# Kernel tuning notes

Measured on AMD Instinct MI355X. Metric: run time of the kernel, lower is better.

The kernel has to match this reference:

```python
import jax, jax.numpy as jnp
import numpy as np

# static config (mirrors init_kwargs)
F_T, S = 8, 24            # video_shape = (F_T, S, S)
K, DIL = 3, 1             # kernel_size, dilation (same for all 3 axes)
HEADS, DHEAD, DIM = 8, 64, 512
INNER = HEADS * DHEAD
PAD = DIL * (K - 1)       # causal: pad 2 at the FRONT of each spatial axis
KJ = K ** 3               # 27 neighbors per query
N_VID = F_T * S * S       # 4608 video tokens


def causal_pad(t):
    # t: [B, D, F, S, S] -> pad front of f/h/w axes (torch F.pad (PAD*?,0) causal layout)
    return jnp.pad(t, ((0, 0), (0, 0), (PAD, 0), (PAD, 0), (PAD, 0)))


def unfold3d(t):
    # torch unfoldNd equivalent. t: [B, D, F+PAD, S+PAD, S+PAD]
    # returns [B, N_VID, KJ, D]; kernel offsets ordered (kf, kh, kw) w fastest,
    # matching torch unfold's channel-major / kernel-minor layout after the
    # rearrange 'b (d j) i -> b i j d'.
    sl = []
    for i in range(K):
        for j in range(K):
            for kk in range(K):
                sl.append(t[:, :, i * DIL:i * DIL + F_T,
                                  j * DIL:j * DIL + S,
                                  kk * DIL:kk * DIL + S])
    u = jnp.stack(sl, axis=2)                      # [B, D, KJ, F, S, S]
    B, D = t.shape[0], t.shape[1]
    u = u.reshape(B, D, KJ, N_VID)
    return jnp.transpose(u, (0, 3, 2, 1))          # [B, N_VID, KJ, D]


def make_mask():
    # True where the neighbor falls into zero padding (out-of-range / future under causal pad)
    ones = jnp.ones((1, 1, F_T, S, S), jnp.float32)
    u = unfold3d(causal_pad(ones))[0, :, :, 0]     # [N_VID, KJ]
    m = u == 0.0
    return jnp.pad(m, ((0, 0), (1, 0)), constant_values=False)  # bos col never masked


def stable_softmax(t, alpha=32.0 ** 2):
    t = t / alpha
    t = t - jax.lax.stop_gradient(jnp.max(t, axis=-1, keepdims=True))
    return jax.nn.softmax(t * alpha, axis=-1)


def setup_inputs() -> dict:
    key = jax.random.key(0)
    ks = jax.random.split(key, 9)
    return {
        "x": jax.random.normal(ks[0], (1, N_VID + 1, DIM), jnp.float32),
        "Wq": jax.random.normal(ks[1], (DIM, INNER), jnp.float32) * 0.02,
        "Wkv": jax.random.normal(ks[2], (DIM, 2 * INNER), jnp.float32) * 0.02,
        "W_th": jax.random.normal(ks[3], (HEADS, HEADS), jnp.float32) * 0.2,
        "Wout": jax.random.normal(ks[4], (INNER, DIM), jnp.float32) * 0.02,
        "bout": jax.random.normal(ks[5], (DIM,), jnp.float32) * 0.02,
        "ax1": jax.random.normal(ks[6], (K, HEADS), jnp.float32),
        "ax2": jax.random.normal(ks[7], (K, HEADS), jnp.float32),
        "ax3": jax.random.normal(ks[8], (K, HEADS), jnp.float32),
    }


def reference(x, Wq, Wkv, W_th, Wout, bout, ax1, ax2, ax3):
    b, n, _ = x.shape                       # b=1, n = 1 + N_VID (no extra padding)
    h, d = HEADS, DHEAD
    scale = d ** -0.5

    q = x @ Wq
    k, v = jnp.split(x @ Wkv, 2, axis=-1)

    def to_heads(t):  # 'b n (h d) -> (b h) n d'
        return t.reshape(b, n, h, d).transpose(0, 2, 1, 3).reshape(b * h, n, d)

    q, k, v = map(to_heads, (q, k, v))
    q = q[:, 1:] * scale                    # drop bos query
    k_bos, v_bos = k[:, :1], v[:, :1]       # [bh, 1, d]
    k, v = k[:, 1:], v[:, 1:]

    def to_vid(t):  # 'b (f h w) d -> b d f h w'
        return t.reshape(b * h, F_T, S, S, d).transpose(0, 4, 1, 2, 3)

    ku = unfold3d(causal_pad(to_vid(k)))    # [bh, N, KJ, d]
    vu = unfold3d(causal_pad(to_vid(v)))
    N = ku.shape[1]

    kb = jnp.broadcast_to(k_bos[:, :, None, :], (b * h, N, 1, d))
    vb = jnp.broadcast_to(v_bos[:, :, None, :], (b * h, N, 1, d))
    ku = jnp.concatenate([kb, ku], axis=2)  # [bh, N, KJ+1, d]
    vu = jnp.concatenate([vb, vu], axis=2)

    sim = jnp.einsum('bid,bijd->bij', q, ku)                 # [bh, N, KJ+1]

    # axial relative position bias over the 3x3x3 kernel, pad 0 for bos column
    rel = (ax1[:, None, None, :] + ax2[None, :, None, :] + ax3[None, None, :, :])
    rel = rel.reshape(KJ, h)                                 # [27, h]
    bias = jnp.pad(rel.T[:, None, :], ((0, 0), (0, 0), (1, 0)))  # [h, 1, KJ+1]

    sim = sim.reshape(b, h, N, KJ + 1) + bias[None]
    mask = make_mask()                                       # [N, KJ+1]
    sim = jnp.where(mask[None, None], -jnp.finfo(sim.dtype).max, sim)

    attn = stable_softmax(sim)                               # [b, h, N, KJ+1]
    attn = jnp.einsum('hg,bgij->bhij', W_th, attn)           # talking heads 1x1 conv

    out = jnp.einsum('bhij,bhijd->bhid', attn, vu.reshape(b, h, N, KJ + 1, d))
    out = jnp.concatenate([v_bos.reshape(b, h, 1, d), out], axis=2)  # re-attach bos value
    out = out.transpose(0, 2, 1, 3).reshape(b, n, h * d)     # '(b h) n d -> b n (h d)'
    return out @ Wout + bout
```

## Files before the change

### kernel.cpp

```cpp
#include <hip/hip_runtime.h>
#include <hip/hip_bf16.h>


constexpr int TFR   = 8;
constexpr int SDIM  = 24;
constexpr int NVID  = TFR * SDIM * SDIM;
constexpr int NTOK  = NVID + 1;
constexpr int NH    = 8;
constexpr int DM    = 512;
constexpr int NJ    = 28;

typedef __attribute__((ext_vector_type(8))) short bf16x8;
typedef __attribute__((ext_vector_type(8))) unsigned short ushort8;
typedef __attribute__((ext_vector_type(4))) float f32x4;

typedef const __attribute__((address_space(1))) unsigned int* gas_ptr;
typedef __attribute__((address_space(3))) unsigned int* las_ptr;

__device__ __forceinline__ float bf2f(unsigned short u) {
    return __uint_as_float((unsigned)u << 16);
}
__device__ __forceinline__ unsigned short f2bf(float f) {
    __hip_bfloat16 h = __float2bfloat16(f);
    return reinterpret_cast<unsigned short&>(h);
}

__global__ __launch_bounds__(256)
void prep_w(const float* __restrict__ Wq, const float* __restrict__ Wkv,
            const float* __restrict__ Wout, const float* __restrict__ x,
            __hip_bfloat16* __restrict__ Wqkvt, __hip_bfloat16* __restrict__ Woutt,
            __hip_bfloat16* __restrict__ xb)
{
    const int tid = threadIdx.x;
    int tb = blockIdx.x;

    if (tb >= 1024) {
        const size_t base = (size_t)(tb - 1024) * 2048 + (size_t)tid * 8;
        if (base < (size_t)NTOK * DM) {
            const float4 f0 = *(const float4*)(x + base);
            const float4 f1 = *(const float4*)(x + base + 4);
            unsigned short v[8] = { f2bf(f0.x), f2bf(f0.y), f2bf(f0.z), f2bf(f0.w),
                                    f2bf(f1.x), f2bf(f1.y), f2bf(f1.z), f2bf(f1.w) };
            *(ushort8*)(xb + base) = *(const ushort8*)v;
        }
        return;
    }

    __shared__ float t[32][33];
    const float* W; __hip_bfloat16* Wt; int Nd, tX, rowOff;
    if (tb < 256)      { W = Wq;   Wt = Wqkvt; Nd = 512;  tX = 16; rowOff = 0;   }
    else if (tb < 768) { tb -= 256; W = Wkv;  Wt = Wqkvt; Nd = 1024; tX = 32; rowOff = 512; }
    else               { tb -= 768; W = Wout; Wt = Woutt; Nd = 512;  tX = 16; rowOff = 0;   }
    const int n0 = (tb % tX) * 32, k0 = (tb / tX) * 32;
    const int r  = tid >> 3;
    const int c4 = (tid & 7) * 4;
    const float4 v = *(const float4*)(W + (size_t)(k0 + r) * Nd + n0 + c4);
    t[r][c4 + 0] = v.x; t[r][c4 + 1] = v.y; t[r][c4 + 2] = v.z; t[r][c4 + 3] = v.w;
    __syncthreads();
    #pragma unroll
    for (int j = 0; j < 4; ++j)
        Wt[(size_t)(rowOff + n0 + r) * 512 + k0 + c4 + j] = __float2bfloat16(t[c4 + j][r]);
}

__global__ __launch_bounds__(256)
void gemm_qkv(const __hip_bfloat16* __restrict__ Ab, const __hip_bfloat16* __restrict__ Bt,
              float* __restrict__ Cq, __hip_bfloat16* __restrict__ Ckv, int M)
{
    constexpr int BM = 128, BN = 128, BK = 64, K = 512;
    __shared__ __align__(16) short As[BM * BK];
    __shared__ __align__(16) short Bs[BN * BK];

    const int tid  = threadIdx.x;
    const int bid  = blockIdx.x;
    const int xcd  = bid & 7, pos = bid >> 3;
    const int L    = (xcd < 4) ? xcd * 56 + pos : 224 + (xcd - 4) * 55 + pos;
    const int m0   = (L / 12) * BM;
    const int n0   = (L % 12) * BN;

    const int lane = tid & 63;
    const int wave = tid >> 6;
    const int wm   = (wave >> 1) * 64;
    const int wn   = (wave & 1) * 64;
    const int col  = lane & 15;
    const int quad = lane >> 4;

    f32x4 acc[4][4] = {};

    for (int k0 = 0; k0 < K; k0 += BK) {
        #pragma unroll
        for (int it = 0; it < 4; ++it) {
            const int idx = it * 256 + tid;
            const int r   = idx >> 3;
            const int u   = (idx & 7) ^ (r & 7);
            const int gm  = (m0 + r < M) ? (m0 + r) : (M - 1);
            const __hip_bfloat16* gp = Ab + (size_t)gm * K + k0 + u * 8;
            __builtin_amdgcn_global_load_lds(
                (gas_ptr)gp, (las_ptr)&As[(it * 256 + wave * 64) * 8], 16, 0, 0);
        }
        #pragma unroll
        for (int it = 0; it < 4; ++it) {
            const int idx = it * 256 + tid;
            const int r   = idx >> 3;
            const int u   = (idx & 7) ^ (r & 7);
            const __hip_bfloat16* gp = Bt + (size_t)(n0 + r) * K + k0 + u * 8;
            __builtin_amdgcn_global_load_lds(
                (gas_ptr)gp, (las_ptr)&Bs[(it * 256 + wave * 64) * 8], 16, 0, 0);
        }
        __syncthreads();

        #pragma unroll
        for (int ks = 0; ks < 2; ++ks) {
            bf16x8 af[4], bfr[4];
            #pragma unroll
            for (int mt = 0; mt < 4; ++mt) {
                const int r = wm + mt * 16 + col;
                const int u = (ks * 4 + quad) ^ (r & 7);
                af[mt] = *(const bf16x8*)(&As[r * BK + u * 8]);
            }
            #pragma unroll
            for (int nt = 0; nt < 4; ++nt) {
                const int r = wn + nt * 16 + col;
                const int u = (ks * 4 + quad) ^ (r & 7);
                bfr[nt] = *(const bf16x8*)(&Bs[r * BK + u * 8]);
            }
            #pragma unroll
            for (int mt = 0; mt < 4; ++mt)
                #pragma unroll
                for (int nt = 0; nt < 4; ++nt)
                    acc[mt][nt] = __builtin_amdgcn_mfma_f32_16x16x32_bf16(
                        af[mt], bfr[nt], acc[mt][nt], 0, 0, 0);
        }
        __syncthreads();
    }

    const bool isQ = (n0 < 512);
    #pragma unroll
    for (int mt = 0; mt < 4; ++mt) {
        #pragma unroll
        for (int r = 0; r < 4; ++r) {
            const int row = m0 + wm + mt * 16 + quad * 4 + r;
            if (row >= M) continue;
            #pragma unroll
            for (int nt = 0; nt < 4; ++nt) {
                const int cg = n0 + wn + nt * 16 + col;
                const float v = acc[mt][nt][r];
                if (isQ) Cq[(size_t)row * 512 + cg] = v * 0.125f;
                else     Ckv[(size_t)row * 1024 + (cg - 512)] = __float2bfloat16(v);
            }
        }
    }
}

__global__ __launch_bounds__(256)
void gemm_out(const __hip_bfloat16* __restrict__ A, const __hip_bfloat16* __restrict__ Bt,
              float* __restrict__ C, int M, const float* __restrict__ bias)
{
    constexpr int BM = 64, BN = 64, BK = 64, K = 512;
    __shared__ __align__(16) short As[BM * BK];
    __shared__ __align__(16) short Bs[BN * BK];

    const int tid  = threadIdx.x;
    const int bid  = blockIdx.x;
    const int L    = (bid & 7) * 73 + (bid >> 3);
    const int m0   = (L >> 3) * BM;
    const int n0   = (L & 7) * BN;
    const int lane = tid & 63;
    const int wave = tid >> 6;
    const int wm   = (wave >> 1) * 32;
    const int wn   = (wave & 1) * 32;
    const int col  = lane & 15;
    const int quad = lane >> 4;

    f32x4 acc[2][2] = {};

    for (int k0 = 0; k0 < K; k0 += BK) {
        #pragma unroll
        for (int it = 0; it < 2; ++it) {
            const int idx = it * 256 + tid;
            const int r   = idx >> 3;
            const int u   = (idx & 7) ^ (r & 7);
            const int gm  = (m0 + r < M) ? (m0 + r) : (M - 1);
            const __hip_bfloat16* gp = A + (size_t)gm * K + k0 + u * 8;
            __builtin_amdgcn_global_load_lds(
                (gas_ptr)gp, (las_ptr)&As[(it * 256 + wave * 64) * 8], 16, 0, 0);
        }
        #pragma unroll
        for (int it = 0; it < 2; ++it) {
            const int idx = it * 256 + tid;
            const int r   = idx >> 3;
            const int u   = (idx & 7) ^ (r & 7);
            const __hip_bfloat16* gp = Bt + (size_t)(n0 + r) * K + k0 + u * 8;
            __builtin_amdgcn_global_load_lds(
                (gas_ptr)gp, (las_ptr)&Bs[(it * 256 + wave * 64) * 8], 16, 0, 0);
        }
        __syncthreads();

        #pragma unroll
        for (int ks = 0; ks < 2; ++ks) {
            bf16x8 af[2], bfr[2];
            #pragma unroll
            for (int mt = 0; mt < 2; ++mt) {
                const int r = wm + mt * 16 + col;
                const int u = (ks * 4 + quad) ^ (r & 7);
                af[mt] = *(const bf16x8*)(&As[r * BK + u * 8]);
            }
            #pragma unroll
            for (int nt = 0; nt < 2; ++nt) {
                const int r = wn + nt * 16 + col;
                const int u = (ks * 4 + quad) ^ (r & 7);
                bfr[nt] = *(const bf16x8*)(&Bs[r * BK + u * 8]);
            }
            #pragma unroll
            for (int mt = 0; mt < 2; ++mt)
                #pragma unroll
                for (int nt = 0; nt < 2; ++nt)
                    acc[mt][nt] = __builtin_amdgcn_mfma_f32_16x16x32_bf16(
                        af[mt], bfr[nt], acc[mt][nt], 0, 0, 0);
        }
        __syncthreads();
    }

    #pragma unroll
    for (int mt = 0; mt < 2; ++mt) {
        #pragma unroll
        for (int r = 0; r < 4; ++r) {
            const int row = m0 + wm + mt * 16 + quad * 4 + r;
            if (row >= M) continue;
            #pragma unroll
            for (int nt = 0; nt < 2; ++nt) {
                const int cg = n0 + wn + nt * 16 + col;
                C[(size_t)row * 512 + cg] = acc[mt][nt][r] + bias[cg];
            }
        }
    }
}

__global__ __launch_bounds__(256)
void attn_v2(const float* __restrict__ Q, const __hip_bfloat16* __restrict__ KVb,
             __hip_bfloat16* __restrict__ O,
             const float* __restrict__ W_th,
             const float* __restrict__ ax1, const float* __restrict__ ax2,
             const float* __restrict__ ax3)
{
    __shared__ float attn_s[4][NH * NJ];
    __shared__ float mixed_s[4][NH * NJ];

    const int tid  = threadIdx.x;
    const int wave = tid >> 6;
    const int lane = tid & 63;
    const int g    = lane >> 3;
    const int s    = lane & 7;
    const int bsw  = (blockIdx.x & 7) * (NVID / 4 / 8) + (blockIdx.x >> 3);
    const int i    = __builtin_amdgcn_readfirstlane(bsw * 4 + (tid >> 6));
    const int qrow = i + 1;

    const int t  = i / (SDIM * SDIM);
    const int rm = i % (SDIM * SDIM);
    const int y  = rm / SDIM;
    const int x  = rm % SDIM;

    float qf[8];
    {
        const float4 q0 = *(const float4*)(Q + (size_t)qrow * DM + lane * 8);
        const float4 q1 = *(const float4*)(Q + (size_t)qrow * DM + lane * 8 + 4);
        qf[0] = q0.x; qf[1] = q0.y; qf[2] = q0.z; qf[3] = q0.w;
        qf[4] = q1.x; qf[5] = q1.y; qf[6] = q1.z; qf[7] = q1.w;
    }
    float a1[3], a2[3], a3[3];
    #pragma unroll
    for (int d = 0; d < 3; ++d) {
        a1[d] = ax1[d * NH + g];
        a2[d] = ax2[d * NH + g];
        a3[d] = ax3[d * NH + g];
    }

    float sim[NJ];
    #pragma unroll
    for (int j = 0; j < NJ; ++j) {
        int row; bool valid; float bias;
        if (j == 0) { row = 0; valid = true; bias = 0.f; }
        else {
            const int jp = j - 1;
            const int di = jp / 9, dj = (jp / 3) % 3, dk = jp % 3;
            const int tt = t + di - 2, yy = y + dj - 2, xx = x + dk - 2;
            valid = (tt >= 0) && (yy >= 0) && (xx >= 0);
            row = 1 + tt * SDIM * SDIM + yy * SDIM + xx;
            bias = a1[di] + a2[dj] + a3[dk];
        }
        if (valid) {
            const ushort8 kv = *(const ushort8*)(KVb + (size_t)row * 1024 + lane * 8);
            float p = 0.f;
            #pragma unroll
            for (int e = 0; e < 8; ++e) p += bf2f(kv[e]) * qf[e];
            p += __shfl_xor(p, 1);
            p += __shfl_xor(p, 2);
            p += __shfl_xor(p, 4);
            sim[j] = p + bias;
        } else {
            sim[j] = -1e30f;
        }
    }

    float m = -1e30f;
    #pragma unroll
    for (int j = 0; j < NJ; ++j) m = fmaxf(m, sim[j]);
    float ssum = 0.f;
    #pragma unroll
    for (int j = 0; j < NJ; ++j) { sim[j] = __expf(sim[j] - m); ssum += sim[j]; }
    const float inv = 1.f / ssum;
    #pragma unroll
    for (int j = 0; j < NJ; ++j) sim[j] *= inv;

    if (s == 0) {
        #pragma unroll
        for (int u = 0; u < 7; ++u) {
            f32x4 v4 = { sim[4*u], sim[4*u+1], sim[4*u+2], sim[4*u+3] };
            *(f32x4*)(&attn_s[wave][g * NJ + 4 * u]) = v4;
        }
    }
    __syncthreads();

    if (tid < NH * NJ) {
        const int h = tid / NJ, j = tid % NJ;
        #pragma unroll
        for (int q = 0; q < 4; ++q) {
            float acc = 0.f;
            #pragma unroll
            for (int gg = 0; gg < NH; ++gg)
                acc += W_th[h * NH + gg] * attn_s[q][gg * NJ + j];
            mixed_s[q][h * NJ + j] = acc;
        }
    }
    __syncthreads();

    float acc8[8] = {};
    #pragma unroll
    for (int j = 0; j < NJ; ++j) {
        int row; bool valid;
        if (j == 0) { row = 0; valid = true; }
        else {
            const int jp = j - 1;
            const int di = jp / 9, dj = (jp / 3) % 3, dk = jp % 3;
            const int tt = t + di - 2, yy = y + dj - 2, xx = x + dk - 2;
            valid = (tt >= 0) && (yy >= 0) && (xx >= 0);
            row = 1 + tt * SDIM * SDIM + yy * SDIM + xx;
        }
        if (valid) {
            const ushort8 vv = *(const ushort8*)(KVb + (size_t)row * 1024 + 512 + lane * 8);
            const float w = mixed_s[wave][g * NJ + j];
            #pragma unroll
            for (int e = 0; e < 8; ++e) acc8[e] += w * bf2f(vv[e]);
        }
    }

    unsigned short o[8];
    #pragma unroll
    for (int e = 0; e < 8; ++e) o[e] = f2bf(acc8[e]);
    *(ushort8*)(O + (size_t)qrow * DM + lane * 8) = *(const ushort8*)o;

    if (i == 0) {
        const ushort8 vb = *(const ushort8*)(KVb + 512 + lane * 8);
        *(ushort8*)(O + lane * 8) = vb;
    }
}

extern "C" void kernel_launch(void* const* d_in, const int* in_sizes, int n_in,
                              void* d_out, int out_size, void* d_ws, size_t ws_size,
                              hipStream_t stream)
{
    const float* x    = (const float*)d_in[0];
    const float* Wq   = (const float*)d_in[1];
    const float* Wkv  = (const float*)d_in[2];
    const float* W_th = (const float*)d_in[3];
    const float* Wout = (const float*)d_in[4];
    const float* bout = (const float*)d_in[5];
    const float* ax1  = (const float*)d_in[6];
    const float* ax2  = (const float*)d_in[7];
    const float* ax3  = (const float*)d_in[8];
    float* out = (float*)d_out;

    char* p = (char*)d_ws;
    float* Qf = (float*)p;                       p += (size_t)NTOK * DM * 4;
    __hip_bfloat16* KVb   = (__hip_bfloat16*)p;  p += (size_t)NTOK * 2 * DM * 2;
    __hip_bfloat16* Ob    = (__hip_bfloat16*)p;  p += (size_t)NTOK * DM * 2;
    __hip_bfloat16* Wqkvt = (__hip_bfloat16*)p;  p += (size_t)3 * DM * DM * 2;
    __hip_bfloat16* Woutt = (__hip_bfloat16*)p;  p += (size_t)DM * DM * 2;
    __hip_bfloat16* xb    = (__hip_bfloat16*)p;  p += (size_t)NTOK * DM * 2;

    const dim3 blk(256);

    prep_w<<<2177, blk, 0, stream>>>(Wq, Wkv, Wout, x, Wqkvt, Woutt, xb);

    gemm_qkv<<<444, blk, 0, stream>>>(xb, Wqkvt, Qf, KVb, NTOK);

    attn_v2<<<dim3(NVID / 4), blk, 0, stream>>>(Qf, KVb, Ob, W_th, ax1, ax2, ax3);

    gemm_out<<<584, blk, 0, stream>>>(Ob, Woutt, out, NTOK, bout);
}
```

Before: 131.1 us.

## Double-buffer LDS tiles in QKV and output GEMMs to overlap loads

Both GEMM kernels now keep two LDS buffers per operand. The next K-tile is issued with global_load_lds into the spare buffer while MFMAs run on the current one, which is meant to hide global-load latency behind compute. LDS use per block doubles, which can lower occupancy, and the loop keeps a single end-of-iteration barrier, so correctness depends on that barrier also waiting for the async LDS loads.

```diff
diff --git a/kernel.cpp b/kernel.cpp
--- a/kernel.cpp
+++ b/kernel.cpp
@@ -67,8 +67,8 @@
               float* __restrict__ Cq, __hip_bfloat16* __restrict__ Ckv, int M)
 {
     constexpr int BM = 128, BN = 128, BK = 64, K = 512;
-    __shared__ __align__(16) short As[BM * BK];
-    __shared__ __align__(16) short Bs[BN * BK];
+    __shared__ __align__(16) short As[2][BM * BK];
+    __shared__ __align__(16) short Bs[2][BN * BK];
 
     const int tid  = threadIdx.x;
     const int bid  = blockIdx.x;
@@ -86,7 +86,7 @@
 
     f32x4 acc[4][4] = {};
 
-    for (int k0 = 0; k0 < K; k0 += BK) {
+    auto stage = [&](int buf, int k0) {
         #pragma unroll
         for (int it = 0; it < 4; ++it) {
             const int idx = it * 256 + tid;
@@ -95,7 +95,7 @@
             const int gm  = (m0 + r < M) ? (m0 + r) : (M - 1);
             const __hip_bfloat16* gp = Ab + (size_t)gm * K + k0 + u * 8;
             __builtin_amdgcn_global_load_lds(
-                (gas_ptr)gp, (las_ptr)&As[(it * 256 + wave * 64) * 8], 16, 0, 0);
+                (gas_ptr)gp, (las_ptr)&As[buf][(it * 256 + wave * 64) * 8], 16, 0, 0);
         }
         #pragma unroll
         for (int it = 0; it < 4; ++it) {
@@ -104,9 +104,17 @@
             const int u   = (idx & 7) ^ (r & 7);
             const __hip_bfloat16* gp = Bt + (size_t)(n0 + r) * K + k0 + u * 8;
             __builtin_amdgcn_global_load_lds(
-                (gas_ptr)gp, (las_ptr)&Bs[(it * 256 + wave * 64) * 8], 16, 0, 0);
-        }
-        __syncthreads();
+                (gas_ptr)gp, (las_ptr)&Bs[buf][(it * 256 + wave * 64) * 8], 16, 0, 0);
+        }
+    };
+
+    stage(0, 0);
+    __syncthreads();
+
+    #pragma unroll 2
+    for (int t = 0; t < K / BK; ++t) {
+        const int cur = t & 1;
+        if (t + 1 < K / BK) stage(cur ^ 1, (t + 1) * BK);
 
         #pragma unroll
         for (int ks = 0; ks < 2; ++ks) {
@@ -115,13 +123,13 @@
             for (int mt = 0; mt < 4; ++mt) {
                 const int r = wm + mt * 16 + col;
                 const int u = (ks * 4 + quad) ^ (r & 7);
-                af[mt] = *(const bf16x8*)(&As[r * BK + u * 8]);
+                af[mt] = *(const bf16x8*)(&As[cur][r * BK + u * 8]);
             }
             #pragma unroll
             for (int nt = 0; nt < 4; ++nt) {
                 const int r = wn + nt * 16 + col;
                 const int u = (ks * 4 + quad) ^ (r & 7);
-                bfr[nt] = *(const bf16x8*)(&Bs[r * BK + u * 8]);
+                bfr[nt] = *(const bf16x8*)(&Bs[cur][r * BK + u * 8]);
             }
             #pragma unroll
             for (int mt = 0; mt < 4; ++mt)
@@ -156,8 +164,8 @@
               float* __restrict__ C, int M, const float* __restrict__ bias)
 {
     constexpr int BM = 64, BN = 64, BK = 64, K = 512;
-    __shared__ __align__(16) short As[BM * BK];
-    __shared__ __align__(16) short Bs[BN * BK];
+    __shared__ __align__(16) short As[2][BM * BK];
+    __shared__ __align__(16) short Bs[2][BN * BK];
 
     const int tid  = threadIdx.x;
     const int bid  = blockIdx.x;
@@ -173,7 +181,7 @@
 
     f32x4 acc[2][2] = {};
 
-    for (int k0 = 0; k0 < K; k0 += BK) {
+    auto stage = [&](int buf, int k0) {
         #pragma unroll
         for (int it = 0; it < 2; ++it) {
             const int idx = it * 256 + tid;
@@ -182,7 +190,7 @@
             const int gm  = (m0 + r < M) ? (m0 + r) : (M - 1);
             const __hip_bfloat16* gp = A + (size_t)gm * K + k0 + u * 8;
             __builtin_amdgcn_global_load_lds(
-                (gas_ptr)gp, (las_ptr)&As[(it * 256 + wave * 64) * 8], 16, 0, 0);
+                (gas_ptr)gp, (las_ptr)&As[buf][(it * 256 + wave * 64) * 8], 16, 0, 0);
         }
         #pragma unroll
         for (int it = 0; it < 2; ++it) {
@@ -191,9 +199,17 @@
             const int u   = (idx & 7) ^ (r & 7);
             const __hip_bfloat16* gp = Bt + (size_t)(n0 + r) * K + k0 + u * 8;
             __builtin_amdgcn_global_load_lds(
-                (gas_ptr)gp, (las_ptr)&Bs[(it * 256 + wave * 64) * 8], 16, 0, 0);
-        }
-        __syncthreads();
+                (gas_ptr)gp, (las_ptr)&Bs[buf][(it * 256 + wave * 64) * 8], 16, 0, 0);
+        }
+    };
+
+    stage(0, 0);
+    __syncthreads();
+
+    #pragma unroll 2
+    for (int t = 0; t < K / BK; ++t) {
+        const int cur = t & 1;
+        if (t + 1 < K / BK) stage(cur ^ 1, (t + 1) * BK);
 
         #pragma unroll
         for (int ks = 0; ks < 2; ++ks) {
@@ -202,13 +218,13 @@
             for (int mt = 0; mt < 2; ++mt) {
                 const int r = wm + mt * 16 + col;
                 const int u = (ks * 4 + quad) ^ (r & 7);
-                af[mt] = *(const bf16x8*)(&As[r * BK + u * 8]);
+                af[mt] = *(const bf16x8*)(&As[cur][r * BK + u * 8]);
             }
             #pragma unroll
             for (int nt = 0; nt < 2; ++nt) {
                 const int r = wn + nt * 16 + col;
                 const int u = (ks * 4 + quad) ^ (r & 7);
-                bfr[nt] = *(const bf16x8*)(&Bs[r * BK + u * 8]);
+                bfr[nt] = *(const bf16x8*)(&Bs[cur][r * BK + u * 8]);
             }
             #pragma unroll
             for (int mt = 0; mt < 2; ++mt)
```

After: 132.2 us. About the same (+0.8%).

## Fuse all four stages into one persistent cooperative kernel with grid syncs

Applied to the files above, without the earlier changes.

Replaces the four separate launches (weight/x prep, QKV GEMM, neighborhood attention, output GEMM) with a single persistent cooperative kernel. Blocks loop over virtual block indices for each stage and separate the stages with grid.sync. The aim is to remove per-launch overhead and inter-kernel gaps. In exchange, stages become grid-strided loops with a grid size set by occupancy, launch_bounds now asks for 3 blocks per CU, the XCD-aware block swizzles are dropped, and the extra __syncthreads and grid barriers add their own cost.

```diff
diff --git a/kernel.cpp b/kernel.cpp
--- a/kernel.cpp
+++ b/kernel.cpp
@@ -1,5 +1,8 @@
 #include <hip/hip_runtime.h>
 #include <hip/hip_bf16.h>
+#include <hip/hip_cooperative_groups.h>
+
+namespace cg = cooperative_groups;
 
 
 constexpr int TFR   = 8;
@@ -25,342 +28,336 @@
     return reinterpret_cast<unsigned short&>(h);
 }
 
-__global__ __launch_bounds__(256)
-void prep_w(const float* __restrict__ Wq, const float* __restrict__ Wkv,
-            const float* __restrict__ Wout, const float* __restrict__ x,
-            __hip_bfloat16* __restrict__ Wqkvt, __hip_bfloat16* __restrict__ Woutt,
-            __hip_bfloat16* __restrict__ xb)
+__global__ __launch_bounds__(256, 3)
+void fused_all(const float* __restrict__ x,   const float* __restrict__ Wq,
+               const float* __restrict__ Wkv,  const float* __restrict__ W_th,
+               const float* __restrict__ Wout, const float* __restrict__ bout,
+               const float* __restrict__ ax1,  const float* __restrict__ ax2,
+               const float* __restrict__ ax3,  float* __restrict__ out,
+               float* __restrict__ Qf, __hip_bfloat16* __restrict__ KVb,
+               __hip_bfloat16* __restrict__ Ob, __hip_bfloat16* __restrict__ Wqkvt,
+               __hip_bfloat16* __restrict__ Woutt, __hip_bfloat16* __restrict__ xb)
 {
-    const int tid = threadIdx.x;
-    int tb = blockIdx.x;
-
-    if (tb >= 1024) {
-        const size_t base = (size_t)(tb - 1024) * 2048 + (size_t)tid * 8;
-        if (base < (size_t)NTOK * DM) {
-            const float4 f0 = *(const float4*)(x + base);
-            const float4 f1 = *(const float4*)(x + base + 4);
-            unsigned short v[8] = { f2bf(f0.x), f2bf(f0.y), f2bf(f0.z), f2bf(f0.w),
-                                    f2bf(f1.x), f2bf(f1.y), f2bf(f1.z), f2bf(f1.w) };
-            *(ushort8*)(xb + base) = *(const ushort8*)v;
-        }
-        return;
-    }
-
-    __shared__ float t[32][33];
-    const float* W; __hip_bfloat16* Wt; int Nd, tX, rowOff;
-    if (tb < 256)      { W = Wq;   Wt = Wqkvt; Nd = 512;  tX = 16; rowOff = 0;   }
-    else if (tb < 768) { tb -= 256; W = Wkv;  Wt = Wqkvt; Nd = 1024; tX = 32; rowOff = 512; }
-    else               { tb -= 768; W = Wout; Wt = Woutt; Nd = 512;  tX = 16; rowOff = 0;   }
-    const int n0 = (tb % tX) * 32, k0 = (tb / tX) * 32;
-    const int r  = tid >> 3;
-    const int c4 = (tid & 7) * 4;
-    const float4 v = *(const float4*)(W + (size_t)(k0 + r) * Nd + n0 + c4);
-    t[r][c4 + 0] = v.x; t[r][c4 + 1] = v.y; t[r][c4 + 2] = v.z; t[r][c4 + 3] = v.w;
-    __syncthreads();
-    #pragma unroll
-    for (int j = 0; j < 4; ++j)
-        Wt[(size_t)(rowOff + n0 + r) * 512 + k0 + c4 + j] = __float2bfloat16(t[c4 + j][r]);
-}
-
-__global__ __launch_bounds__(256)
-void gemm_qkv(const __hip_bfloat16* __restrict__ Ab, const __hip_bfloat16* __restrict__ Bt,
-              float* __restrict__ Cq, __hip_bfloat16* __restrict__ Ckv, int M)
-{
-    constexpr int BM = 128, BN = 128, BK = 64, K = 512;
-    __shared__ __align__(16) short As[BM * BK];
-    __shared__ __align__(16) short Bs[BN * BK];
-
+    __shared__ __align__(16) char smem[32768];
     const int tid  = threadIdx.x;
-    const int bid  = blockIdx.x;
-    const int xcd  = bid & 7, pos = bid >> 3;
-    const int L    = (xcd < 4) ? xcd * 56 + pos : 224 + (xcd - 4) * 55 + pos;
-    const int m0   = (L / 12) * BM;
-    const int n0   = (L % 12) * BN;
-
+    const int nblk = gridDim.x;
     const int lane = tid & 63;
     const int wave = tid >> 6;
-    const int wm   = (wave >> 1) * 64;
-    const int wn   = (wave & 1) * 64;
     const int col  = lane & 15;
     const int quad = lane >> 4;
-
-    f32x4 acc[4][4] = {};
-
-    for (int k0 = 0; k0 < K; k0 += BK) {
-        #pragma unroll
-        for (int it = 0; it < 4; ++it) {
-            const int idx = it * 256 + tid;
-            const int r   = idx >> 3;
-            const int u   = (idx & 7) ^ (r & 7);
-            const int gm  = (m0 + r < M) ? (m0 + r) : (M - 1);
-            const __hip_bfloat16* gp = Ab + (size_t)gm * K + k0 + u * 8;
-            __builtin_amdgcn_global_load_lds(
-                (gas_ptr)gp, (las_ptr)&As[(it * 256 + wave * 64) * 8], 16, 0, 0);
-        }
-        #pragma unroll
-        for (int it = 0; it < 4; ++it) {
-            const int idx = it * 256 + tid;
-            const int r   = idx >> 3;
-            const int u   = (idx & 7) ^ (r & 7);
-            const __hip_bfloat16* gp = Bt + (size_t)(n0 + r) * K + k0 + u * 8;
-            __builtin_amdgcn_global_load_lds(
-                (gas_ptr)gp, (las_ptr)&Bs[(it * 256 + wave * 64) * 8], 16, 0, 0);
-        }
-        __syncthreads();
-
-        #pragma unroll
-        for (int ks = 0; ks < 2; ++ks) {
-            bf16x8 af[4], bfr[4];
-            #pragma unroll
-            for (int mt = 0; mt < 4; ++mt) {
-                const int r = wm + mt * 16 + col;
-                const int u = (ks * 4 + quad) ^ (r & 7);
-                af[mt] = *(const bf16x8*)(&As[r * BK + u * 8]);
-            }
-            #pragma unroll
-            for (int nt = 0; nt < 4; ++nt) {
-                const int r = wn + nt * 16 + col;
-                const int u = (ks * 4 + quad) ^ (r & 7);
-                bfr[nt] = *(const bf16x8*)(&Bs[r * BK + u * 8]);
-            }
-            #pragma unroll
-            for (int mt = 0; mt < 4; ++mt)
-                #pragma unroll
-                for (int nt = 0; nt < 4; ++nt)
-                    acc[mt][nt] = __builtin_amdgcn_mfma_f32_16x16x32_bf16(
-                        af[mt], bfr[nt], acc[mt][nt], 0, 0, 0);
-        }
-        __syncthreads();
-    }
-
-    const bool isQ = (n0 < 512);
-    #pragma unroll
-    for (int mt = 0; mt < 4; ++mt) {
-        #pragma unroll
-        for (int r = 0; r < 4; ++r) {
-            const int row = m0 + wm + mt * 16 + quad * 4 + r;
-            if (row >= M) continue;
-            #pragma unroll
-            for (int nt = 0; nt < 4; ++nt) {
-                const int cg = n0 + wn + nt * 16 + col;
-                const float v = acc[mt][nt][r];
-                if (isQ) Cq[(size_t)row * 512 + cg] = v * 0.125f;
-                else     Ckv[(size_t)row * 1024 + (cg - 512)] = __float2bfloat16(v);
-            }
+    cg::grid_group grid = cg::this_grid();
+
+    for (int vb = blockIdx.x; vb < 2177; vb += nblk) {
+        if (vb >= 1024) {
+            const size_t base = (size_t)(vb - 1024) * 2048 + (size_t)tid * 8;
+            if (base < (size_t)NTOK * DM) {
+                const float4 f0 = *(const float4*)(x + base);
+                const float4 f1 = *(const float4*)(x + base + 4);
+                unsigned short v[8] = { f2bf(f0.x), f2bf(f0.y), f2bf(f0.z), f2bf(f0.w),
+                                        f2bf(f1.x), f2bf(f1.y), f2bf(f1.z), f2bf(f1.w) };
+                *(ushort8*)(xb + base) = *(const ushort8*)v;
+            }
+        } else {
+            float (*t)[33] = reinterpret_cast<float(*)[33]>(smem);
+            int tb = vb;
+            const float* W; __hip_bfloat16* Wt; int Nd, tX, rowOff;
+            if (tb < 256)      { W = Wq;   Wt = Wqkvt; Nd = 512;  tX = 16; rowOff = 0;   }
+            else if (tb < 768) { tb -= 256; W = Wkv;  Wt = Wqkvt; Nd = 1024; tX = 32; rowOff = 512; }
+            else               { tb -= 768; W = Wout; Wt = Woutt; Nd = 512;  tX = 16; rowOff = 0;   }
+            const int n0 = (tb % tX) * 32, k0 = (tb / tX) * 32;
+            const int r  = tid >> 3;
+            const int c4 = (tid & 7) * 4;
+            const float4 v = *(const float4*)(W + (size_t)(k0 + r) * Nd + n0 + c4);
+            __syncthreads();
+            t[r][c4 + 0] = v.x; t[r][c4 + 1] = v.y; t[r][c4 + 2] = v.z; t[r][c4 + 3] = v.w;
+            __syncthreads();
+            #pragma unroll
+            for (int j = 0; j < 4; ++j)
+                Wt[(size_t)(rowOff + n0 + r) * 512 + k0 + c4 + j] = __float2bfloat16(t[c4 + j][r]);
         }
     }
-}
-
-__global__ __launch_bounds__(256)
-void gemm_out(const __hip_bfloat16* __restrict__ A, const __hip_bfloat16* __restrict__ Bt,
-              float* __restrict__ C, int M, const float* __restrict__ bias)
-{
-    constexpr int BM = 64, BN = 64, BK = 64, K = 512;
-    __shared__ __align__(16) short As[BM * BK];
-    __shared__ __align__(16) short Bs[BN * BK];
-
-    const int tid  = threadIdx.x;
-    const int bid  = blockIdx.x;
-    const int L    = (bid & 7) * 73 + (bid >> 3);
-    const int m0   = (L >> 3) * BM;
-    const int n0   = (L & 7) * BN;
-    const int lane = tid & 63;
-    const int wave = tid >> 6;
-    const int wm   = (wave >> 1) * 32;
-    const int wn   = (wave & 1) * 32;
-    const int col  = lane & 15;
-    const int quad = lane >> 4;
-
-    f32x4 acc[2][2] = {};
-
-    for (int k0 = 0; k0 < K; k0 += BK) {
-        #pragma unroll
-        for (int it = 0; it < 2; ++it) {
-            const int idx = it * 256 + tid;
-            const int r   = idx >> 3;
-            const int u   = (idx & 7) ^ (r & 7);
-            const int gm  = (m0 + r < M) ? (m0 + r) : (M - 1);
-            const __hip_bfloat16* gp = A + (size_t)gm * K + k0 + u * 8;
-            __builtin_amdgcn_global_load_lds(
-                (gas_ptr)gp, (las_ptr)&As[(it * 256 + wave * 64) * 8], 16, 0, 0);
-        }
-        #pragma unroll
-        for (int it = 0; it < 2; ++it) {
-            const int idx = it * 256 + tid;
-            const int r   = idx >> 3;
-            const int u   = (idx & 7) ^ (r & 7);
-            const __hip_bfloat16* gp = Bt + (size_t)(n0 + r) * K + k0 + u * 8;
-            __builtin_amdgcn_global_load_lds(
-                (gas_ptr)gp, (las_ptr)&Bs[(it * 256 + wave * 64) * 8], 16, 0, 0);
-        }
-        __syncthreads();
-
-        #pragma unroll
-        for (int ks = 0; ks < 2; ++ks) {
-            bf16x8 af[2], bfr[2];
-            #pragma unroll
-            for (int mt = 0; mt < 2; ++mt) {
-                const int r = wm + mt * 16 + col;
-                const int u = (ks * 4 + quad) ^ (r & 7);
-                af[mt] = *(const bf16x8*)(&As[r * BK + u * 8]);
-            }
-            #pragma unroll
-            for (int nt = 0; nt < 2; ++nt) {
-                const int r = wn + nt * 16 + col;
-                const int u = (ks * 4 + quad) ^ (r & 7);
-                bfr[nt] = *(const bf16x8*)(&Bs[r * BK + u * 8]);
-            }
-            #pragma unroll
-            for (int mt = 0; mt < 2; ++mt)
-                #pragma unroll
-                for (int nt = 0; nt < 2; ++nt)
-                    acc[mt][nt] = __builtin_amdgcn_mfma_f32_16x16x32_bf16(
-                        af[mt], bfr[nt], acc[mt][nt], 0, 0, 0);
-        }
-        __syncthreads();
-    }
-
-    #pragma unroll
-    for (int mt = 0; mt < 2; ++mt) {
-        #pragma unroll
-        for (int r = 0; r < 4; ++r) {
-            const int row = m0 + wm + mt * 16 + quad * 4 + r;
-            if (row >= M) continue;
-            #pragma unroll
-            for (int nt = 0; nt < 2; ++nt) {
-                const int cg = n0 + wn + nt * 16 + col;
-                C[(size_t)row * 512 + cg] = acc[mt][nt][r] + bias[cg];
+    __threadfence();
+    grid.sync();
+    __threadfence();
+
+    {
+        short* As = (short*)smem;
+        short* Bs = (short*)(smem + 16384);
+        const int wm = (wave >> 1) * 64;
+        const int wn = (wave & 1) * 64;
+
+        for (int vb = blockIdx.x; vb < 444; vb += nblk) {
+            const int m0 = (vb / 12) * 128;
+            const int n0 = (vb % 12) * 128;
+
+            f32x4 acc[4][4] = {};
+
+            for (int k0 = 0; k0 < 512; k0 += 64) {
+                #pragma unroll
+                for (int it = 0; it < 4; ++it) {
+                    const int idx = it * 256 + tid;
+                    const int r   = idx >> 3;
+                    const int u   = (idx & 7) ^ (r & 7);
+                    const int gm  = (m0 + r < NTOK) ? (m0 + r) : (NTOK - 1);
+                    __builtin_amdgcn_global_load_lds(
+                        (gas_ptr)(xb + (size_t)gm * 512 + k0 + u * 8),
+                        (las_ptr)&As[(it * 256 + wave * 64) * 8], 16, 0, 0);
+                }
+                #pragma unroll
+                for (int it = 0; it < 4; ++it) {
+                    const int idx = it * 256 + tid;
+                    const int r   = idx >> 3;
+                    const int u   = (idx & 7) ^ (r & 7);
+                    __builtin_amdgcn_global_load_lds(
+                        (gas_ptr)(Wqkvt + (size_t)(n0 + r) * 512 + k0 + u * 8),
+                        (las_ptr)&Bs[(it * 256 + wave * 64) * 8], 16, 0, 0);
+                }
+                __syncthreads();
+
+                #pragma unroll
+                for (int ks = 0; ks < 2; ++ks) {
+                    bf16x8 af[4], bfr[4];
+                    #pragma unroll
+                    for (int mt = 0; mt < 4; ++mt) {
+                        const int r = wm + mt * 16 + col;
+                        const int u = (ks * 4 + quad) ^ (r & 7);
+                        af[mt] = *(const bf16x8*)(&As[r * 64 + u * 8]);
+                    }
+                    #pragma unroll
+                    for (int nt = 0; nt < 4; ++nt) {
+                        const int r = wn + nt * 16 + col;
+                        const int u = (ks * 4 + quad) ^ (r & 7);
+                        bfr[nt] = *(const bf16x8*)(&Bs[r * 64 + u * 8]);
+                    }
+                    #pragma unroll
+                    for (int mt = 0; mt < 4; ++mt)
+                        #pragma unroll
+                        for (int nt = 0; nt < 4; ++nt)
+                            acc[mt][nt] = __builtin_amdgcn_mfma_f32_16x16x32_bf16(
+                                af[mt], bfr[nt], acc[mt][nt], 0, 0, 0);
+                }
+                __syncthreads();
+            }
+
+            const bool isQ = (n0 < 512);
+            #pragma unroll
+            for (int mt = 0; mt < 4; ++mt) {
+                #pragma unroll
+                for (int r = 0; r < 4; ++r) {
+                    const int row = m0 + wm + mt * 16 + quad * 4 + r;
+                    if (row >= NTOK) continue;
+                    #pragma unroll
+                    for (int nt = 0; nt < 4; ++nt) {
+                        const int cg = n0 + wn + nt * 16 + col;
+                        const float v = acc[mt][nt][r];
+                        if (isQ) Qf[(size_t)row * 512 + cg] = v * 0.125f;
+                        else     KVb[(size_t)row * 1024 + (cg - 512)] = __float2bfloat16(v);
+                    }
+                }
             }
         }
     }
-}
-
-__global__ __launch_bounds__(256)
-void attn_v2(const float* __restrict__ Q, const __hip_bfloat16* __restrict__ KVb,
-             __hip_bfloat16* __restrict__ O,
-             const float* __restrict__ W_th,
-             const float* __restrict__ ax1, const float* __restrict__ ax2,
-             const float* __restrict__ ax3)
-{
-    __shared__ float attn_s[4][NH * NJ];
-    __shared__ float mixed_s[4][NH * NJ];
-
-    const int tid  = threadIdx.x;
-    const int wave = tid >> 6;
-    const int lane = tid & 63;
-    const int g    = lane >> 3;
-    const int s    = lane & 7;
-    const int bsw  = (blockIdx.x & 7) * (NVID / 4 / 8) + (blockIdx.x >> 3);
-    const int i    = __builtin_amdgcn_readfirstlane(bsw * 4 + (tid >> 6));
-    const int qrow = i + 1;
-
-    const int t  = i / (SDIM * SDIM);
-    const int rm = i % (SDIM * SDIM);
-    const int y  = rm / SDIM;
-    const int x  = rm % SDIM;
-
-    float qf[8];
+    __threadfence();
+    grid.sync();
+    __threadfence();
+
     {
-        const float4 q0 = *(const float4*)(Q + (size_t)qrow * DM + lane * 8);
-        const float4 q1 = *(const float4*)(Q + (size_t)qrow * DM + lane * 8 + 4);
-        qf[0] = q0.x; qf[1] = q0.y; qf[2] = q0.z; qf[3] = q0.w;
-        qf[4] = q1.x; qf[5] = q1.y; qf[6] = q1.z; qf[7] = q1.w;
-    }
-    float a1[3], a2[3], a3[3];
-    #pragma unroll
-    for (int d = 0; d < 3; ++d) {
-        a1[d] = ax1[d * NH + g];
-        a2[d] = ax2[d * NH + g];
-        a3[d] = ax3[d * NH + g];
-    }
-
-    float sim[NJ];
-    #pragma unroll
-    for (int j = 0; j < NJ; ++j) {
-        int row; bool valid; float bias;
-        if (j == 0) { row = 0; valid = true; bias = 0.f; }
-        else {
-            const int jp = j - 1;
-            const int di = jp / 9, dj = (jp / 3) % 3, dk = jp % 3;
-            const int tt = t + di - 2, yy = y + dj - 2, xx = x + dk - 2;
-            valid = (tt >= 0) && (yy >= 0) && (xx >= 0);
-            row = 1 + tt * SDIM * SDIM + yy * SDIM + xx;
-            bias = a1[di] + a2[dj] + a3[dk];
-        }
-        if (valid) {
-            const ushort8 kv = *(const ushort8*)(KVb + (size_t)row * 1024 + lane * 8);
-            float p = 0.f;
-            #pragma unroll
-            for (int e = 0; e < 8; ++e) p += bf2f(kv[e]) * qf[e];
-            p += __shfl_xor(p, 1);
-            p += __shfl_xor(p, 2);
-            p += __shfl_xor(p, 4);
-            sim[j] = p + bias;
-        } else {
-            sim[j] = -1e30f;
+        float* attn_s  = (float*)smem;
+        float* mixed_s = (float*)(smem + 3584);
+        const int g = lane >> 3;
+        const int s = lane & 7;
+
+        for (int vb = blockIdx.x; vb < NVID / 4; vb += nblk) {
+            const int i    = __builtin_amdgcn_readfirstlane(vb * 4 + wave);
+            const int qrow = i + 1;
+            const int t  = i / (SDIM * SDIM);
+            const int rm = i % (SDIM * SDIM);
+            const int y  = rm / SDIM;
+            const int xq = rm % SDIM;
+
+            float qf[8];
+            {
+                const float4 q0 = *(const float4*)(Qf + (size_t)qrow * DM + lane * 8);
+                const float4 q1 = *(const float4*)(Qf + (size_t)qrow * DM + lane * 8 + 4);
+                qf[0] = q0.x; qf[1] = q0.y; qf[2] = q0.z; qf[3] = q0.w;
+                qf[4] = q1.x; qf[5] = q1.y; qf[6] = q1.z; qf[7] = q1.w;
+            }
+            float a1[3], a2[3], a3[3];
+            #pragma unroll
+            for (int d = 0; d < 3; ++d) {
+                a1[d] = ax1[d * NH + g];
+                a2[d] = ax2[d * NH + g];
+                a3[d] = ax3[d * NH + g];
+            }
+
+            float sim[NJ];
+            #pragma unroll
+            for (int j = 0; j < NJ; ++j) {
+                int row; bool valid; float bias;
+                if (j == 0) { row = 0; valid = true; bias = 0.f; }
+                else {
+                    const int jp = j - 1;
+                    const int di = jp / 9, dj = (jp / 3) % 3, dk = jp % 3;
+                    const int tt = t + di - 2, yy = y + dj - 2, xx = xq + dk - 2;
+                    valid = (tt >= 0) && (yy >= 0) && (xx >= 0);
+                    row = 1 + tt * SDIM * SDIM + yy * SDIM + xx;
+                    bias = a1[di] + a2[dj] + a3[dk];
+                }
+                if (valid) {
+                    const ushort8 kv = *(const ushort8*)(KVb + (size_t)row * 1024 + lane * 8);
+                    float p = 0.f;
+                    #pragma unroll
+                    for (int e = 0; e < 8; ++e) p += bf2f(kv[e]) * qf[e];
+                    p += __shfl_xor(p, 1);
+                    p += __shfl_xor(p, 2);
+                    p += __shfl_xor(p, 4);
+                    sim[j] = p + bias;
+                } else {
+                    sim[j] = -1e30f;
+                }
+            }
+
+            float m = -1e30f;
+            #pragma unroll
+            for (int j = 0; j < NJ; ++j) m = fmaxf(m, sim[j]);
+            float ssum = 0.f;
+            #pragma unroll
+            for (int j = 0; j < NJ; ++j) { sim[j] = __expf(sim[j] - m); ssum += sim[j]; }
+            const float inv = 1.f / ssum;
+            #pragma unroll
+            for (int j = 0; j < NJ; ++j) sim[j] *= inv;
+
+            if (s == 0) {
+                #pragma unroll
+                for (int u = 0; u < 7; ++u) {
+                    f32x4 v4 = { sim[4*u], sim[4*u+1], sim[4*u+2], sim[4*u+3] };
+                    *(f32x4*)(&attn_s[wave * (NH * NJ) + g * NJ + 4 * u]) = v4;
+                }
+            }
+            __syncthreads();
+
+            if (tid < NH * NJ) {
+                const int h = tid / NJ, j = tid % NJ;
+                #pragma unroll
+                for (int q = 0; q < 4; ++q) {
+                    float acc = 0.f;
+                    #pragma unroll
+                    for (int gg = 0; gg < NH; ++gg)
+                        acc += W_th[h * NH + gg] * attn_s[q * (NH * NJ) + gg * NJ + j];
+                    mixed_s[q * (NH * NJ) + h * NJ + j] = acc;
+                }
+            }
+            __syncthreads();
+
+            float acc8[8] = {};
+            #pragma unroll
+            for (int j = 0; j < NJ; ++j) {
+                int row; bool valid;
+                if (j == 0) { row = 0; valid = true; }
+                else {
+                    const int jp = j - 1;
+                    const int di = jp / 9, dj = (jp / 3) % 3, dk = jp % 3;
+                    const int tt = t + di - 2, yy = y + dj - 2, xx = xq + dk - 2;
+                    valid = (tt >= 0) && (yy >= 0) && (xx >= 0);
+                    row = 1 + tt * SDIM * SDIM + yy * SDIM + xx;
+                }
+                if (valid) {
+                    const ushort8 vv = *(const ushort8*)(KVb + (size_t)row * 1024 + 512 + lane * 8);
+                    const float w = mixed_s[wave * (NH * NJ) + g * NJ + j];
+                    #pragma unroll
+                    for (int e = 0; e < 8; ++e) acc8[e] += w * bf2f(vv[e]);
+                }
+            }
+
+            unsigned short o[8];
+            #pragma unroll
+            for (int e = 0; e < 8; ++e) o[e] = f2bf(acc8[e]);
+            *(ushort8*)(Ob + (size_t)qrow * DM + lane * 8) = *(const ushort8*)o;
+
+            if (i == 0) {
+                const ushort8 vb0 = *(const ushort8*)(KVb + 512 + lane * 8);
+                *(ushort8*)(Ob + lane * 8) = vb0;
+            }
+            __syncthreads();
         }
     }
-
-    float m = -1e30f;
-    #pragma unroll
-    for (int j = 0; j < NJ; ++j) m = fmaxf(m, sim[j]);
-    float ssum = 0.f;
-    #pragma unroll
-    for (int j = 0; j < NJ; ++j) { sim[j] = __expf(sim[j] - m); ssum += sim[j]; }
-    const float inv = 1.f / ssum;
-    #pragma unroll
-    for (int j = 0; j < NJ; ++j) sim[j] *= inv;
-
-    if (s == 0) {
-        #pragma unroll
-        for (int u = 0; u < 7; ++u) {
-            f32x4 v4 = { sim[4*u], sim[4*u+1], sim[4*u+2], sim[4*u+3] };
-            *(f32x4*)(&attn_s[wave][g * NJ + 4 * u]) = v4;
+    __threadfence();
+    grid.sync();
+    __threadfence();
+
+    {
+        short* As = (short*)smem;
+        short* Bs = (short*)(smem + 8192);
+        const int wm = (wave >> 1) * 32;
+        const int wn = (wave & 1) * 32;
+
+        for (int vb = blockIdx.x; vb < 584; vb += nblk) {
+            const int m0 = (vb >> 3) * 64;
+            const int n0 = (vb & 7) * 64;
+
+            f32x4 acc[2][2] = {};
+
+            for (int k0 = 0; k0 < 512; k0 += 64) {
+                #pragma unroll
+                for (int it = 0; it < 2; ++it) {
+                    const int idx = it * 256 + tid;
+                    const int r   = idx >> 3;
+                    const int u   = (idx & 7) ^ (r & 7);
+                    const int gm  = (m0 + r < NTOK) ? (m0 + r) : (NTOK - 1);
+                    __builtin_amdgcn_global_load_lds(
+                        (gas_ptr)(Ob + (size_t)gm * 512 + k0 + u * 8),
+                        (las_ptr)&As[(it * 256 + wave * 64) * 8], 16, 0, 0);
+                }
+                #pragma unroll
+                for (int it = 0; it < 2; ++it) {
+                    const int idx = it * 256 + tid;
+                    const int r   = idx >> 3;
+                    const int u   = (idx & 7) ^ (r & 7);
+                    __builtin_amdgcn_global_load_lds(
+                        (gas_ptr)(Woutt + (size_t)(n0 + r) * 512 + k0 + u * 8),
+                        (las_ptr)&Bs[(it * 256 + wave * 64) * 8], 16, 0, 0);
+                }
+                __syncthreads();
+
+                #pragma unroll
+                for (int ks = 0; ks < 2; ++ks) {
+                    bf16x8 af[2], bfr[2];
+                    #pragma unroll
+                    for (int mt = 0; mt < 2; ++mt) {
+                        const int r = wm + mt * 16 + col;
+                        const int u = (ks * 4 + quad) ^ (r & 7);
+                        af[mt] = *(const bf16x8*)(&As[r * 64 + u * 8]);
+                    }
+                    #pragma unroll
+                    for (int nt = 0; nt < 2; ++nt) {
+                        const int r = wn + nt * 16 + col;
+                        const int u = (ks * 4 + quad) ^ (r & 7);
+                        bfr[nt] = *(const bf16x8*)(&Bs[r * 64 + u * 8]);
+                    }
+                    #pragma unroll
+                    for (int mt = 0; mt < 2; ++mt)
+                        #pragma unroll
+                        for (int nt = 0; nt < 2; ++nt)
+                            acc[mt][nt] = __builtin_amdgcn_mfma_f32_16x16x32_bf16(
+                                af[mt], bfr[nt], acc[mt][nt], 0, 0, 0);
+                }
+                __syncthreads();
+            }
+
+            #pragma unroll
+            for (int mt = 0; mt < 2; ++mt) {
+                #pragma unroll
+                for (int r = 0; r < 4; ++r) {
+                    const int row = m0 + wm + mt * 16 + quad * 4 + r;
+                    if (row >= NTOK) continue;
+                    #pragma unroll
+                    for (int nt = 0; nt < 2; ++nt) {
+                        const int cg = n0 + wn + nt * 16 + col;
+                        out[(size_t)row * 512 + cg] = acc[mt][nt][r] + bout[cg];
+                    }
+                }
+            }
         }
-    }
-    __syncthreads();
-
-    if (tid < NH * NJ) {
-        const int h = tid / NJ, j = tid % NJ;
-        #pragma unroll
-        for (int q = 0; q < 4; ++q) {
-            float acc = 0.f;
-            #pragma unroll
-            for (int gg = 0; gg < NH; ++gg)
-                acc += W_th[h * NH + gg] * attn_s[q][gg * NJ + j];
-            mixed_s[q][h * NJ + j] = acc;
-        }
-    }
-    __syncthreads();
-
-    float acc8[8] = {};
-    #pragma unroll
-    for (int j = 0; j < NJ; ++j) {
-        int row; bool valid;
-        if (j == 0) { row = 0; valid = true; }
-        else {
-            const int jp = j - 1;
-            const int di = jp / 9, dj = (jp / 3) % 3, dk = jp % 3;
-            const int tt = t + di - 2, yy = y + dj - 2, xx = x + dk - 2;
-            valid = (tt >= 0) && (yy >= 0) && (xx >= 0);
-            row = 1 + tt * SDIM * SDIM + yy * SDIM + xx;
-        }
-        if (valid) {
-            const ushort8 vv = *(const ushort8*)(KVb + (size_t)row * 1024 + 512 + lane * 8);
-            const float w = mixed_s[wave][g * NJ + j];
-            #pragma unroll
-            for (int e = 0; e < 8; ++e) acc8[e] += w * bf2f(vv[e]);
-        }
-    }
-
-    unsigned short o[8];
-    #pragma unroll
-    for (int e = 0; e < 8; ++e) o[e] = f2bf(acc8[e]);
-    *(ushort8*)(O + (size_t)qrow * DM + lane * 8) = *(const ushort8*)o;
-
-    if (i == 0) {
-        const ushort8 vb = *(const ushort8*)(KVb + 512 + lane * 8);
-        *(ushort8*)(O + lane * 8) = vb;
     }
 }
 
@@ -387,13 +384,22 @@
     __hip_bfloat16* Woutt = (__hip_bfloat16*)p;  p += (size_t)DM * DM * 2;
     __hip_bfloat16* xb    = (__hip_bfloat16*)p;  p += (size_t)NTOK * DM * 2;
 
-    const dim3 blk(256);
-
-    prep_w<<<2177, blk, 0, stream>>>(Wq, Wkv, Wout, x, Wqkvt, Woutt, xb);
-
-    gemm_qkv<<<444, blk, 0, stream>>>(xb, Wqkvt, Qf, KVb, NTOK);
-
-    attn_v2<<<dim3(NVID / 4), blk, 0, stream>>>(Qf, KVb, Ob, W_th, ax1, ax2, ax3);
-
-    gemm_out<<<584, blk, 0, stream>>>(Ob, Woutt, out, NTOK, bout);
+    static int gridBlocks = 0;
+    if (gridBlocks == 0) {
+        int nb = 0;
+        hipOccupancyMaxActiveBlocksPerMultiprocessor(
+            &nb, reinterpret_cast<const void*>(&fused_all), 256, 0);
+        if (nb < 1) nb = 1;
+        gridBlocks = nb * 256;
+        if (gridBlocks > 1152) gridBlocks = 1152;
+    }
+
+    void* kargs[] = {
+        (void*)&x,   (void*)&Wq,   (void*)&Wkv,  (void*)&W_th,
+        (void*)&Wout,(void*)&bout, (void*)&ax1,  (void*)&ax2,
+        (void*)&ax3, (void*)&out,  (void*)&Qf,   (void*)&KVb,
+        (void*)&Ob,  (void*)&Wqkvt,(void*)&Woutt,(void*)&xb
+    };
+    hipLaunchCooperativeKernel(reinterpret_cast<void*>(&fused_all),
+                               dim3(gridBlocks), dim3(256), kargs, 0, stream);
 }
```

After: 415.1 us. 217% more time.

## Halve QKV GEMM M-tile and do talking-heads mixing via wave shuffles

Applied to the files above, without the earlier changes.

The QKV GEMM tile height drops from 128 to 64 rows and the grid grows from 444 to 876 blocks, giving more parallelism across CUs on this moderately sized problem. Separately, the attention kernel no longer mixes heads through shared memory with two block-wide barriers. Each lane now reads its own row of W_th and gathers the other heads' softmax weights with xor-shuffles across the 8 lane groups. This removes the LDS traffic and barriers but adds many cross-lane shuffles and register pressure from the 28-entry mix array.

```diff
diff --git a/kernel.cpp b/kernel.cpp
--- a/kernel.cpp
+++ b/kernel.cpp
@@ -66,29 +66,29 @@
 void gemm_qkv(const __hip_bfloat16* __restrict__ Ab, const __hip_bfloat16* __restrict__ Bt,
               float* __restrict__ Cq, __hip_bfloat16* __restrict__ Ckv, int M)
 {
-    constexpr int BM = 128, BN = 128, BK = 64, K = 512;
+    constexpr int BM = 64, BN = 128, BK = 64, K = 512;
     __shared__ __align__(16) short As[BM * BK];
     __shared__ __align__(16) short Bs[BN * BK];
 
     const int tid  = threadIdx.x;
     const int bid  = blockIdx.x;
     const int xcd  = bid & 7, pos = bid >> 3;
-    const int L    = (xcd < 4) ? xcd * 56 + pos : 224 + (xcd - 4) * 55 + pos;
+    const int L    = (xcd < 4) ? xcd * 110 + pos : 440 + (xcd - 4) * 109 + pos;
     const int m0   = (L / 12) * BM;
     const int n0   = (L % 12) * BN;
 
     const int lane = tid & 63;
     const int wave = tid >> 6;
-    const int wm   = (wave >> 1) * 64;
+    const int wm   = (wave >> 1) * 32;
     const int wn   = (wave & 1) * 64;
     const int col  = lane & 15;
     const int quad = lane >> 4;
 
-    f32x4 acc[4][4] = {};
+    f32x4 acc[2][4] = {};
 
     for (int k0 = 0; k0 < K; k0 += BK) {
         #pragma unroll
-        for (int it = 0; it < 4; ++it) {
+        for (int it = 0; it < 2; ++it) {
             const int idx = it * 256 + tid;
             const int r   = idx >> 3;
             const int u   = (idx & 7) ^ (r & 7);
@@ -110,9 +110,9 @@
 
         #pragma unroll
         for (int ks = 0; ks < 2; ++ks) {
-            bf16x8 af[4], bfr[4];
-            #pragma unroll
-            for (int mt = 0; mt < 4; ++mt) {
+            bf16x8 af[2], bfr[4];
+            #pragma unroll
+            for (int mt = 0; mt < 2; ++mt) {
                 const int r = wm + mt * 16 + col;
                 const int u = (ks * 4 + quad) ^ (r & 7);
                 af[mt] = *(const bf16x8*)(&As[r * BK + u * 8]);
@@ -124,7 +124,7 @@
                 bfr[nt] = *(const bf16x8*)(&Bs[r * BK + u * 8]);
             }
             #pragma unroll
-            for (int mt = 0; mt < 4; ++mt)
+            for (int mt = 0; mt < 2; ++mt)
                 #pragma unroll
                 for (int nt = 0; nt < 4; ++nt)
                     acc[mt][nt] = __builtin_amdgcn_mfma_f32_16x16x32_bf16(
@@ -135,7 +135,7 @@
 
     const bool isQ = (n0 < 512);
     #pragma unroll
-    for (int mt = 0; mt < 4; ++mt) {
+    for (int mt = 0; mt < 2; ++mt) {
         #pragma unroll
         for (int r = 0; r < 4; ++r) {
             const int row = m0 + wm + mt * 16 + quad * 4 + r;
@@ -242,14 +242,9 @@
              const float* __restrict__ ax1, const float* __restrict__ ax2,
              const float* __restrict__ ax3)
 {
-    __shared__ float attn_s[4][NH * NJ];
-    __shared__ float mixed_s[4][NH * NJ];
-
     const int tid  = threadIdx.x;
-    const int wave = tid >> 6;
     const int lane = tid & 63;
     const int g    = lane >> 3;
-    const int s    = lane & 7;
     const int bsw  = (blockIdx.x & 7) * (NVID / 4 / 8) + (blockIdx.x >> 3);
     const int i    = __builtin_amdgcn_readfirstlane(bsw * 4 + (tid >> 6));
     const int qrow = i + 1;
@@ -273,6 +268,9 @@
         a2[d] = ax2[d * NH + g];
         a3[d] = ax3[d * NH + g];
     }
+    float w_row[8];
+    #pragma unroll
+    for (int k = 0; k < 8; ++k) w_row[k] = W_th[g * NH + k];
 
     float sim[NJ];
     #pragma unroll
@@ -311,27 +309,16 @@
     #pragma unroll
     for (int j = 0; j < NJ; ++j) sim[j] *= inv;
 
-    if (s == 0) {
-        #pragma unroll
-        for (int u = 0; u < 7; ++u) {
-            f32x4 v4 = { sim[4*u], sim[4*u+1], sim[4*u+2], sim[4*u+3] };
-            *(f32x4*)(&attn_s[wave][g * NJ + 4 * u]) = v4;
-        }
-    }
-    __syncthreads();
-
-    if (tid < NH * NJ) {
-        const int h = tid / NJ, j = tid % NJ;
-        #pragma unroll
-        for (int q = 0; q < 4; ++q) {
-            float acc = 0.f;
-            #pragma unroll
-            for (int gg = 0; gg < NH; ++gg)
-                acc += W_th[h * NH + gg] * attn_s[q][gg * NJ + j];
-            mixed_s[q][h * NJ + j] = acc;
-        }
-    }
-    __syncthreads();
+    float mix[NJ];
+    #pragma unroll
+    for (int j = 0; j < NJ; ++j) mix[j] = w_row[g] * sim[j];
+    #pragma unroll
+    for (int k = 1; k < 8; ++k) {
+        const float w = w_row[g ^ k];
+        #pragma unroll
+        for (int j = 0; j < NJ; ++j)
+            mix[j] += w * __shfl_xor(sim[j], k * 8);
+    }
 
     float acc8[8] = {};
     #pragma unroll
@@ -347,7 +334,7 @@
         }
         if (valid) {
             const ushort8 vv = *(const ushort8*)(KVb + (size_t)row * 1024 + 512 + lane * 8);
-            const float w = mixed_s[wave][g * NJ + j];
+            const float w = mix[j];
             #pragma unroll
             for (int e = 0; e < 8; ++e) acc8[e] += w * bf2f(vv[e]);
         }
@@ -391,7 +378,7 @@
 
     prep_w<<<2177, blk, 0, stream>>>(Wq, Wkv, Wout, x, Wqkvt, Woutt, xb);
 
-    gemm_qkv<<<444, blk, 0, stream>>>(xb, Wqkvt, Qf, KVb, NTOK);
+    gemm_qkv<<<876, blk, 0, stream>>>(xb, Wqkvt, Qf, KVb, NTOK);
 
     attn_v2<<<dim3(NVID / 4), blk, 0, stream>>>(Qf, KVb, Ob, W_th, ax1, ax2, ax3);
 
```

Result: slower. 154.9 us (+18.1%).
